# Kernel tuning notes

Hardware: AMD Instinct MI355X
Metric: run time of the kernel (lower is better)

The kernel has to match this reference:

```python
import jax, jax.numpy as jnp
import numpy as np

Tx, V, D = 512, 100, 64
DM, NH, DFF, NL = 512, 8, 2048, 2
H, DATT, FCH, OUT = 256, 128, 256, 2


def setup_inputs() -> dict:
    key = jax.random.key(0)
    ks = jax.random.split(key, 16)
    s = 0.02
    w = lambda k, shape: jax.random.normal(k, shape, jnp.float32) * s
    return dict(
        x_data=jax.random.normal(ks[0], (1, Tx, V, D), jnp.float32),
        feat_w=w(ks[1], (DM, D)), feat_b=jnp.zeros((DM,), jnp.float32),
        in_w=w(ks[2], (NL, 3 * DM, DM)), in_b=jnp.zeros((NL, 3 * DM), jnp.float32),
        out_w=w(ks[3], (NL, DM, DM)), out_b=jnp.zeros((NL, DM), jnp.float32),
        ff1_w=w(ks[4], (NL, DFF, DM)), ff1_b=jnp.zeros((NL, DFF), jnp.float32),
        ff2_w=w(ks[5], (NL, DM, DFF)), ff2_b=jnp.zeros((NL, DM), jnp.float32),
        ln1_g=jnp.ones((NL, DM), jnp.float32), ln1_b=jnp.zeros((NL, DM), jnp.float32),
        ln2_g=jnp.ones((NL, DM), jnp.float32), ln2_b=jnp.zeros((NL, DM), jnp.float32),
        att1_w=w(ks[6], (DATT, DM + H)), att1_b=jnp.zeros((DATT,), jnp.float32),
        att2_w=w(ks[7], (1, DATT)), att2_b=jnp.zeros((1,), jnp.float32),
        lstm_wih=w(ks[8], (4 * H, DM)), lstm_whh=w(ks[9], (4 * H, H)),
        lstm_bih=jnp.zeros((4 * H,), jnp.float32), lstm_bhh=jnp.zeros((4 * H,), jnp.float32),
        fc1_w=w(ks[10], (FCH, DM + H)), fc1_b=jnp.zeros((FCH,), jnp.float32),
        fc2_w=w(ks[11], (OUT, FCH)), fc2_b=jnp.zeros((OUT,), jnp.float32),
    )


def _layernorm(x, g, b):
    m = x.mean(-1, keepdims=True)
    v = x.var(-1, keepdims=True)
    return (x - m) * jax.lax.rsqrt(v + 1e-5) * g + b


def _forward(x_data, feat_w, feat_b, in_w, in_b, out_w, out_b, ff1_w, ff1_b,
             ff2_w, ff2_b, ln1_g, ln1_b, ln2_g, ln2_b, att1_w, att1_b,
             att2_w, att2_b, lstm_wih, lstm_whh, lstm_bih, lstm_bhh,
             fc1_w, fc1_b, fc2_w, fc2_b):
    x = x_data[0]                              # [Tx, V, D]
    x = jnp.swapaxes(x, 0, 1)                  # [V, Tx, D]  (seq=V, batch=Tx)
    x = x @ feat_w.T + feat_b                  # feature mapping -> [V, Tx, DM]
    # sinusoidal positional encoding over the V (seq) axis
    pos = jnp.arange(V, dtype=jnp.float32)[:, None]
    div = jnp.exp(jnp.arange(0, DM, 2, dtype=jnp.float32) * (-np.log(10000.0) / DM))
    pe = jnp.zeros((V, DM), jnp.float32)
    pe = pe.at[:, 0::2].set(jnp.sin(pos * div)).at[:, 1::2].set(jnp.cos(pos * div))
    x = x + pe[:, None, :]
    hd = DM // NH
    for l in range(NL):                        # post-norm TransformerEncoderLayer
        qkv = x @ in_w[l].T + in_b[l]          # [V, Tx, 3*DM]
        q, k, v = jnp.split(qkv, 3, axis=-1)
        q = q.reshape(V, Tx, NH, hd)
        k = k.reshape(V, Tx, NH, hd)
        v = v.reshape(V, Tx, NH, hd)
        scores = jnp.einsum('ibhd,jbhd->bhij', q, k) / np.sqrt(hd).astype(np.float32)
        attn = jax.nn.softmax(scores, axis=-1)
        ctx = jnp.einsum('bhij,jbhd->ibhd', attn, v).reshape(V, Tx, DM)
        x = _layernorm(x + ctx @ out_w[l].T + out_b[l], ln1_g[l], ln1_b[l])
        ff = jax.nn.relu(x @ ff1_w[l].T + ff1_b[l]) @ ff2_w[l].T + ff2_b[l]
        x = _layernorm(x + ff, ln2_g[l], ln2_b[l])
    hs = jnp.swapaxes(x, 0, 1)                 # [Tx, V, DM]

    def step(carry, h_i):                      # h_i: [V, DM]
        s_h, s_c = carry                       # [1, H] each
        att_in = jnp.concatenate([h_i, jnp.broadcast_to(s_h, (V, H))], axis=1)
        a1 = jnp.tanh(att_in @ att1_w.T + att1_b)
        a2 = a1 @ att2_w.T + att2_b            # [V, 1]
        a2 = a2 - jnp.max(a2)
        alpha = jnp.exp(a2)
        alpha = alpha / (jnp.sum(alpha, axis=0, keepdims=True) + 1e-15)
        c = jnp.sum(alpha * h_i, axis=0, keepdims=True)   # [1, DM]
        gates = c @ lstm_wih.T + lstm_bih + s_h @ lstm_whh.T + lstm_bhh
        i_g, f_g, g_g, o_g = jnp.split(gates, 4, axis=-1)
        s_c_new = jax.nn.sigmoid(f_g) * s_c + jax.nn.sigmoid(i_g) * jnp.tanh(g_g)
        s_h_new = jax.nn.sigmoid(o_g) * jnp.tanh(s_c_new)
        fc_in = jnp.concatenate([c, s_h], axis=1)  # uses PREVIOUS hidden, per original
        fc = jax.nn.relu(fc_in @ fc1_w.T + fc1_b) @ fc2_w.T + fc2_b
        log_prob = jax.nn.log_softmax(fc, axis=1)  # [1, OUT]
        return (s_h_new, s_c_new), log_prob

    init = (jnp.zeros((1, H), jnp.float32), jnp.zeros((1, H), jnp.float32))
    _, logs = jax.lax.scan(step, init, hs)
    return logs[-1]                            # last timestep's log-probs [1, OUT]


def reference(x_data, feat_w, feat_b, in_w, in_b, out_w, out_b, ff1_w, ff1_b,
              ff2_w, ff2_b, ln1_g, ln1_b, ln2_g, ln2_b, att1_w, att1_b,
              att2_w, att2_b, lstm_wih, lstm_whh, lstm_bih, lstm_bhh,
              fc1_w, fc1_b, fc2_w, fc2_b):
    return _forward(x_data, feat_w, feat_b, in_w, in_b, out_w, out_b, ff1_w,
                    ff1_b, ff2_w, ff2_b, ln1_g, ln1_b, ln2_g, ln2_b, att1_w,
                    att1_b, att2_w, att2_b, lstm_wih, lstm_whh, lstm_bih,
                    lstm_bhh, fc1_w, fc1_b, fc2_w, fc2_b)
```

## Files before the change

kernel.cpp:

```cpp
#include <hip/hip_runtime.h>
#include <hip/hip_bf16.h>


typedef __attribute__((ext_vector_type(8))) short short8;
typedef __attribute__((ext_vector_type(4))) float f32x4;

__device__ __forceinline__ int jglob_of(int e0, int jl) { return ((jl >> 4) << 8) + e0 + (jl & 15); }
__device__ __forceinline__ float blo(unsigned u) { return __uint_as_float(u << 16); }
__device__ __forceinline__ float bhi(unsigned u) { return __uint_as_float(u & 0xffff0000u); }
__device__ __forceinline__ short f2bs(float x) {
  union { __hip_bfloat16 h; short s; } u; u.h = __float2bfloat16(x); return u.s;
}
__device__ __forceinline__ float tanhf_fast(float x) {
  float e = __expf(2.f * x);
  return 1.f - 2.f * __builtin_amdgcn_rcpf(e + 1.f);
}

#define GLL16(GSRC, LDST) \
  __builtin_amdgcn_global_load_lds( \
      (const __attribute__((address_space(1))) unsigned int*)(GSRC), \
      (__attribute__((address_space(3))) unsigned int*)(LDST), 16, 0, 0)

__global__ __launch_bounds__(256) void pe_kernel(float* __restrict__ pe) {
  int idx = blockIdx.x * 256 + threadIdx.x;
  if (idx >= 100 * 512) return;
  int v = idx >> 9, n = idx & 511;
  float d = expf(-(float)(n & ~1) * (9.2103403719761836f / 512.0f));
  float ang = (float)v * d;
  pe[idx] = (n & 1) ? cosf(ang) : sinf(ang);
}

__global__ __launch_bounds__(256) void cvt2_kernel(const float* __restrict__ src,
                                                   __hip_bfloat16* __restrict__ dst,
                                                   int n, int w, int stride) {
  int i = blockIdx.x * 256 + threadIdx.x;
  if (i < n) dst[i] = __float2bfloat16(src[(i / w) * stride + (i % w)]);
}

__global__ __launch_bounds__(256) void gemm_bf16(
    const __hip_bfloat16* __restrict__ A, long aBase, int aDiv, long aSA, long aSB,
    const __hip_bfloat16* __restrict__ W, int ldw,
    const float* __restrict__ bias,
    float* __restrict__ outF, __hip_bfloat16* __restrict__ outB,
    long oBase, int oDiv, long oSA, long oSB, long oSC,
    int K, int addTo, int relu)
{
  __shared__ __hip_bfloat16 As[128 * 64];
  __shared__ __hip_bfloat16 Bs[128 * 64];
  const int tid = threadIdx.x;
  const int rT = blockIdx.y * 128, nT = blockIdx.x * 128;
  const int wave = tid >> 6, lane = tid & 63;
  const int wr = wave >> 1, wc = wave & 1;
  const int lrow = lane & 15, lkg = lane >> 4;

  long asrc[4], bsrc[4];
  const int sc8 = ((lane & 7) ^ (lane >> 3)) * 8;
#pragma unroll
  for (int i = 0; i < 4; ++i) {
    const int chunk = wave * 4 + i;
    const int row = chunk * 8 + (lane >> 3);
    const int gr = rT + row;
    asrc[i] = aBase + (long)(gr / aDiv) * aSA + (long)(gr % aDiv) * aSB + sc8;
    bsrc[i] = (long)(nT + row) * ldw + sc8;
  }

  f32x4 acc[4][4];
#pragma unroll
  for (int i = 0; i < 4; ++i)
#pragma unroll
    for (int j = 0; j < 4; ++j) acc[i][j] = (f32x4){0.f, 0.f, 0.f, 0.f};

  for (int k0 = 0; k0 < K; k0 += 64) {
#pragma unroll
    for (int i = 0; i < 4; ++i) {
      const int chunk = wave * 4 + i;
      GLL16(A + asrc[i] + k0, &As[chunk * 512]);
      GLL16(W + bsrc[i] + k0, &Bs[chunk * 512]);
    }
    __syncthreads();
#pragma unroll
    for (int ks = 0; ks < 2; ++ks) {
      short8 af[4], bfv[4];
#pragma unroll
      for (int f = 0; f < 4; ++f) {
        const int Ra = wr * 64 + f * 16 + lrow;
        af[f] = *(const short8*)&As[Ra * 64 + (((ks * 4 + lkg) ^ (Ra & 7)) * 8)];
        const int Rb = wc * 64 + f * 16 + lrow;
        bfv[f] = *(const short8*)&Bs[Rb * 64 + (((ks * 4 + lkg) ^ (Rb & 7)) * 8)];
      }
#pragma unroll
      for (int fm = 0; fm < 4; ++fm)
#pragma unroll
        for (int fn = 0; fn < 4; ++fn)
          acc[fm][fn] = __builtin_amdgcn_mfma_f32_16x16x32_bf16(af[fm], bfv[fn], acc[fm][fn], 0, 0, 0);
    }
    __syncthreads();
  }

  float bias_v[4];
#pragma unroll
  for (int fn = 0; fn < 4; ++fn)
    bias_v[fn] = bias ? bias[nT + wc * 64 + fn * 16 + lrow] : 0.f;

#pragma unroll
  for (int fm = 0; fm < 4; ++fm) {
#pragma unroll
    for (int r = 0; r < 4; ++r) {
      const int grow = rT + wr * 64 + fm * 16 + lkg * 4 + r;
      const long obase_r = oBase + (long)(grow / oDiv) * oSA + (long)(grow % oDiv) * oSB;
#pragma unroll
      for (int fn = 0; fn < 4; ++fn) {
        const int gcol = nT + wc * 64 + fn * 16 + lrow;
        float v = acc[fm][fn][r] + bias_v[fn];
        if (relu) v = fmaxf(v, 0.f);
        const long o = obase_r + (long)gcol * oSC;
        if (outF) { if (addTo) v += outF[o]; outF[o] = v; }
        else {
          if (addTo) v += __bfloat162float(outB[o]);
          outB[o] = __float2bfloat16(v);
        }
      }
    }
  }
}

__global__ __launch_bounds__(256) void gemm_mfma(
    const float* __restrict__ A, long aBase, int aDiv, long aSA, long aSB,
    const float* __restrict__ W, int ldw,
    const float* __restrict__ bias,
    const float* __restrict__ extra, int extraDiv,
    __hip_bfloat16* __restrict__ outB,
    long oBase, int oDiv, long oSA, long oSB,
    int N, int K)
{
  __shared__ short As[2][128][40];
  __shared__ short Bs[2][128][40];
  const int tid = threadIdx.x;
  const int rT = blockIdx.y * 128, nT = blockIdx.x * 128;
  const int wave = tid >> 6, lane = tid & 63;
  const int wr = wave >> 1, wc = wave & 1;
  const int lrow = lane & 15, lkg = lane >> 4;
  const int srow = tid >> 1, shf = tid & 1;

  const long arow = aBase + (long)((rT + srow) / aDiv) * aSA + (long)((rT + srow) % aDiv) * aSB + shf * 16;
  const long brow = (long)(nT + srow) * ldw + shf * 16;

  f32x4 acc[4][4];
#pragma unroll
  for (int i = 0; i < 4; ++i)
#pragma unroll
    for (int j = 0; j < 4; ++j) acc[i][j] = (f32x4){0.f, 0.f, 0.f, 0.f};

  float4 ra[4], rb[4];
#define LOADT(K0) do { \
    const float* _pa = A + arow + (K0); \
    ra[0] = *(const float4*)(_pa); ra[1] = *(const float4*)(_pa + 4); \
    ra[2] = *(const float4*)(_pa + 8); ra[3] = *(const float4*)(_pa + 12); \
    const float* _pb = W + brow + (K0); \
    rb[0] = *(const float4*)(_pb); rb[1] = *(const float4*)(_pb + 4); \
    rb[2] = *(const float4*)(_pb + 8); rb[3] = *(const float4*)(_pb + 12); \
  } while (0)

#define CVST(DST, X, Y) do { \
    short8 _v; \
    _v[0] = f2bs((X).x); _v[1] = f2bs((X).y); _v[2] = f2bs((X).z); _v[3] = f2bs((X).w); \
    _v[4] = f2bs((Y).x); _v[5] = f2bs((Y).y); _v[6] = f2bs((Y).z); _v[7] = f2bs((Y).w); \
    *(short8*)(DST) = _v; \
  } while (0)

#define STAGE(BUF) do { \
    CVST(&As[BUF][srow][shf * 16],     ra[0], ra[1]); \
    CVST(&As[BUF][srow][shf * 16 + 8], ra[2], ra[3]); \
    CVST(&Bs[BUF][srow][shf * 16],     rb[0], rb[1]); \
    CVST(&Bs[BUF][srow][shf * 16 + 8], rb[2], rb[3]); \
  } while (0)

  LOADT(0);
  STAGE(0);
  __syncthreads();

  int cur = 0;
  for (int k0 = 0; k0 < K; k0 += 32) {
    const bool nlast = (k0 + 32 < K);
    if (nlast) LOADT(k0 + 32);
    short8 af[4], bfv[4];
#pragma unroll
    for (int f = 0; f < 4; ++f)
      af[f] = *(const short8*)&As[cur][wr * 64 + f * 16 + lrow][lkg * 8];
#pragma unroll
    for (int f = 0; f < 4; ++f)
      bfv[f] = *(const short8*)&Bs[cur][wc * 64 + f * 16 + lrow][lkg * 8];
#pragma unroll
    for (int fm = 0; fm < 4; ++fm)
#pragma unroll
      for (int fn = 0; fn < 4; ++fn)
        acc[fm][fn] = __builtin_amdgcn_mfma_f32_16x16x32_bf16(af[fm], bfv[fn], acc[fm][fn], 0, 0, 0);
    if (nlast) STAGE(cur ^ 1);
    __syncthreads();
    cur ^= 1;
  }

  float bias_v[4];
#pragma unroll
  for (int fn = 0; fn < 4; ++fn)
    bias_v[fn] = bias ? bias[nT + wc * 64 + fn * 16 + lrow] : 0.f;

#pragma unroll
  for (int fm = 0; fm < 4; ++fm) {
#pragma unroll
    for (int r = 0; r < 4; ++r) {
      const int grow = rT + wr * 64 + fm * 16 + lkg * 4 + r;
      const long obase_r = oBase + (long)(grow / oDiv) * oSA + (long)(grow % oDiv) * oSB;
      const long exrow = (long)(grow / extraDiv) * N;
#pragma unroll
      for (int fn = 0; fn < 4; ++fn) {
        const int gcol = nT + wc * 64 + fn * 16 + lrow;
        float v = acc[fm][fn][r] + bias_v[fn];
        if (extra) v += extra[exrow + gcol];
        outB[obase_r + gcol] = __float2bfloat16(v);
      }
    }
  }
#undef LOADT
#undef CVST
#undef STAGE
}

__global__ __launch_bounds__(256) void attn_kernel(
    const __hip_bfloat16* __restrict__ qkv, __hip_bfloat16* __restrict__ outY, int b0)
{
  __shared__ __align__(16) char arena[101632];
  unsigned short* Qs = (unsigned short*)arena;
  unsigned short* Ks = Qs + 8064;
  unsigned short* Vt = Ks + 8064;
  float* S = (float*)(arena + 49664);
  unsigned short* Sb = (unsigned short*)arena;
  __shared__ float rs_s[112];

  const int h = blockIdx.x, bl = blockIdx.y, tid = threadIdx.x;
  const unsigned short* q16 = (const unsigned short*)qkv;

  for (int idx = tid; idx < 6400; idx += 256) {
    int v = idx >> 6, d = idx & 63;
    long base = ((long)(v * 256 + bl)) * 1536 + h * 64 + d;
    Qs[v * 72 + d] = q16[base];
    Ks[v * 72 + d] = q16[base + 512];
    Vt[d * 136 + v] = q16[base + 1024];
  }
  for (int idx = tid; idx < 12 * 64; idx += 256) {
    int r = 100 + (idx >> 6), c = idx & 63;
    Qs[r * 72 + c] = 0; Ks[r * 72 + c] = 0;
  }
  for (int idx = tid; idx < 64 * 36; idx += 256) {
    int d = idx / 36, c = 100 + idx % 36;
    Vt[d * 136 + c] = 0;
  }
  __syncthreads();

  const int wave = tid >> 6, lane = tid & 63;
  const int lrow = lane & 15, lkg = lane >> 4;

  for (int tt = wave; tt < 49; tt += 4) {
    const int tm = tt / 7, tn = tt % 7;
    f32x4 a = (f32x4){0.f, 0.f, 0.f, 0.f};
#pragma unroll
    for (int ks = 0; ks < 2; ++ks) {
      short8 af = *(const short8*)&Qs[(tm * 16 + lrow) * 72 + ks * 32 + lkg * 8];
      short8 bf = *(const short8*)&Ks[(tn * 16 + lrow) * 72 + ks * 32 + lkg * 8];
      a = __builtin_amdgcn_mfma_f32_16x16x32_bf16(af, bf, a, 0, 0, 0);
    }
#pragma unroll
    for (int r = 0; r < 4; ++r)
      S[(tm * 16 + lkg * 4 + r) * 116 + tn * 16 + lrow] = a[r] * 0.125f;
  }
  __syncthreads();

  {
    unsigned* p = (unsigned*)Sb;
    for (int idx = tid; idx < 7616; idx += 256) p[idx] = 0;
  }
  __syncthreads();

  if (tid < 200) {
    const int r = tid >> 1, hf = tid & 1;
    const float* srow = S + r * 116 + hf * 50;
    float m = -3.0e38f;
    for (int c = 0; c < 50; ++c) m = fmaxf(m, srow[c]);
    m = fmaxf(m, __shfl_xor(m, 1, 64));
    float s = 0.f;
    for (int c = 0; c < 50; ++c) {
      float e = __expf(srow[c] - m);
      Sb[r * 136 + hf * 50 + c] = (unsigned short)f2bs(e);
      s += e;
    }
    s += __shfl_xor(s, 1, 64);
    if (hf == 0) rs_s[r] = 1.f / s;
  }
  __syncthreads();

  for (int tt = wave; tt < 28; tt += 4) {
    const int tm = tt >> 2, tn = tt & 3;
    f32x4 a = (f32x4){0.f, 0.f, 0.f, 0.f};
#pragma unroll
    for (int kc = 0; kc < 4; ++kc) {
      short8 af = *(const short8*)&Sb[(tm * 16 + lrow) * 136 + kc * 32 + lkg * 8];
      short8 bf = *(const short8*)&Vt[(tn * 16 + lrow) * 136 + kc * 32 + lkg * 8];
      a = __builtin_amdgcn_mfma_f32_16x16x32_bf16(af, bf, a, 0, 0, 0);
    }
#pragma unroll
    for (int r = 0; r < 4; ++r) {
      const int m = tm * 16 + lkg * 4 + r;
      if (m < 100) {
        const int n = tn * 16 + lrow;
        outY[((long)(m * 512 + b0 + bl)) * 512 + h * 64 + n] = __float2bfloat16(a[r] * rs_s[m]);
      }
    }
  }
}

__global__ __launch_bounds__(256) void ln_kernel(__hip_bfloat16* __restrict__ X,
    const float* __restrict__ g, const float* __restrict__ b)
{
  const int row = blockIdx.x * 4 + (threadIdx.x >> 6);
  const int lane = threadIdx.x & 63;
  unsigned short* x = (unsigned short*)X + (long)row * 512 + lane * 8;
  uint4 raw = *(const uint4*)x;
  float v[8];
  v[0] = blo(raw.x); v[1] = bhi(raw.x); v[2] = blo(raw.y); v[3] = bhi(raw.y);
  v[4] = blo(raw.z); v[5] = bhi(raw.z); v[6] = blo(raw.w); v[7] = bhi(raw.w);
  float s = 0.f, sq = 0.f;
#pragma unroll
  for (int i = 0; i < 8; ++i) { s += v[i]; sq += v[i] * v[i]; }
#pragma unroll
  for (int off = 32; off; off >>= 1) { s += __shfl_xor(s, off, 64); sq += __shfl_xor(sq, off, 64); }
  const float mean = s * (1.f / 512.f);
  const float var = sq * (1.f / 512.f) - mean * mean;
  const float inv = rsqrtf(var + 1e-5f);
  const int c0 = lane * 8;
  short8 outv;
#pragma unroll
  for (int i = 0; i < 8; ++i)
    outv[i] = f2bs((v[i] - mean) * inv * g[c0 + i] + b[c0 + i]);
  *(short8*)x = outv;
}

__global__ void init_kernel(unsigned long long* sh_units, float* c_g) {
  int t = threadIdx.x;
  sh_units[t] = 0ULL;
  sh_units[256 + t] = 0ULL;
  c_g[t] = 0.f; c_g[256 + t] = 0.f;
}

#define DEC_NB 16

__global__ __launch_bounds__(256, 1) void decoder_kernel(
    const __hip_bfloat16* __restrict__ Xb,
    const __hip_bfloat16* __restrict__ Pb,
    const __hip_bfloat16* __restrict__ Gb,
    const float* __restrict__ att1_w, const float* __restrict__ att1_b,
    const float* __restrict__ att2_w,
    const float* __restrict__ whh,
    const float* __restrict__ bih, const float* __restrict__ bhh,
    const float* __restrict__ fc1_w, const float* __restrict__ fc1_b,
    const float* __restrict__ fc2_w, const float* __restrict__ fc2_b,
    unsigned long long* sh_units,
    float* c_g,
    float* __restrict__ out)
{
  if (blockIdx.x & 7) return;
  const int tid = threadIdx.x;
  const int blk = blockIdx.x >> 3;
  const int e0 = blk * 16;

  __shared__ __align__(16) float s_h_s[256];
  __shared__ float w2_s[128], ub_s[128], bsum_s[64];
  __shared__ float u_s[128], sc_s[16];
  __shared__ float a2_s[104];
  __shared__ float red_s[256];
  __shared__ float gates_s[64];
  __shared__ float red4_s[4];
  __shared__ float fcin_s[768];
  __shared__ float fca_s[256];

  if (tid < 128) { w2_s[tid] = att2_w[tid]; ub_s[tid] = att1_b[tid]; }
  if (tid < 64) {
    int jg = jglob_of(e0, tid);
    bsum_s[tid] = bih[jg] + bhh[jg];
  }
  if (tid < 16) sc_s[tid] = 0.f;
  if (tid < 4) a2_s[100 + tid] = 0.f;

  const int pv = tid >> 1, ppart = tid & 1;
  const int pvv = (pv < 100) ? pv : 99;
  const int gjl = tid >> 2, gq = tid & 3;
  const long gRowOff = (long)jglob_of(e0, gjl) * 100 + gq * 26;

  unsigned W1R[64];
  {
    const int j = tid >> 1, hf = tid & 1;
    const float* wsrc = att1_w + (long)j * 768 + 512 + hf * 128;
#pragma unroll
    for (int i = 0; i < 64; ++i)
      W1R[i] = (unsigned)(unsigned short)f2bs(wsrc[2 * i]) |
               ((unsigned)(unsigned short)f2bs(wsrc[2 * i + 1]) << 16);
  }
  float WHF[64];
  {
    const float* wsrc = whh + (long)jglob_of(e0, gjl) * 256 + gq * 64;
#pragma unroll
    for (int i = 0; i < 64; ++i) WHF[i] = wsrc[i];
  }

  unsigned PCa[32], PCb[32];
  unsigned GCa[13], GCb[13];

#define PREFETCH(T1, PCd, GCd) do { \
    const uint4* _pp = (const uint4*)Pb + ((((long)(T1) * 100 + pvv) * 128 + ppart * 64) >> 3); \
    _Pragma("unroll") \
    for (int _i = 0; _i < 8; ++_i) { \
      uint4 _t = _pp[_i]; \
      (PCd)[4*_i] = _t.x; (PCd)[4*_i+1] = _t.y; (PCd)[4*_i+2] = _t.z; (PCd)[4*_i+3] = _t.w; \
    } \
    const unsigned* _gp = (const unsigned*)(Gb + (long)(T1) * 102400 + gRowOff); \
    _Pragma("unroll") \
    for (int _i = 0; _i < 13; ++_i) (GCd)[_i] = _gp[_i]; \
  } while (0)

#define STEP(T, PCc, GCc, PCn, GCn) do { \
    { \
      unsigned long long* _up = &sh_units[((((T) & 1) ^ 1) << 8) + tid]; \
      unsigned long long _v = __hip_atomic_load(_up, __ATOMIC_RELAXED, __HIP_MEMORY_SCOPE_AGENT); \
      while ((unsigned)(_v >> 32) < (unsigned)(T)) { \
        __builtin_amdgcn_s_sleep(1); \
        _v = __hip_atomic_load(_up, __ATOMIC_RELAXED, __HIP_MEMORY_SCOPE_AGENT); \
      } \
      s_h_s[tid] = __uint_as_float((unsigned)_v); \
    } \
    __syncthreads(); \
    if ((T) + 1 < 512) PREFETCH((T) + 1, PCn, GCn); \
    { const int _hf = tid & 1, _j = tid >> 1; \
      const float* _sh = &s_h_s[_hf * 128]; \
      float _a = 0.f; \
      _Pragma("unroll") \
      for (int _i = 0; _i < 64; ++_i) { \
        const unsigned _w = W1R[_i]; \
        const float2 _s2 = *(const float2*)(_sh + 2 * _i); \
        _a += blo(_w) * _s2.x + bhi(_w) * _s2.y; \
      } \
      _a += __shfl_xor(_a, 1, 64); \
      if (_hf == 0) u_s[_j] = _a + ub_s[_j]; \
    } \
    float _hhv; \
    { const float* _sh = &s_h_s[gq * 64]; \
      float _a = 0.f; \
      _Pragma("unroll") \
      for (int _i = 0; _i < 16; ++_i) { \
        const float4 _s4 = *(const float4*)(_sh + 4 * _i); \
        _a += WHF[4*_i] * _s4.x + WHF[4*_i+1] * _s4.y + WHF[4*_i+2] * _s4.z + WHF[4*_i+3] * _s4.w; \
      } \
      _a += __shfl_xor(_a, 1, 64); \
      _a += __shfl_xor(_a, 2, 64); \
      _hhv = _a; \
    } \
    __syncthreads(); \
    { float _val = 0.f; \
      _Pragma("unroll") \
      for (int _jj = 0; _jj < 64; ++_jj) { \
        unsigned _u = (PCc)[_jj >> 1]; \
        float _pf = (_jj & 1) ? bhi(_u) : blo(_u); \
        int _col = ppart * 64 + _jj; \
        _val += tanhf_fast(_pf + u_s[_col]) * w2_s[_col]; \
      } \
      _val += __shfl_xor(_val, 1, 64); \
      if (ppart == 0 && pv < 100) a2_s[pv] = _val; \
    } \
    __syncthreads(); \
    if (tid < 64) { \
      float _x0 = a2_s[tid]; \
      float _x1 = (tid + 64 < 100) ? a2_s[tid + 64] : -3.0e38f; \
      float _m = fmaxf(_x0, _x1); \
      _Pragma("unroll") \
      for (int _o = 32; _o; _o >>= 1) _m = fmaxf(_m, __shfl_xor(_m, _o, 64)); \
      float _e0 = __expf(_x0 - _m); \
      float _e1 = (tid + 64 < 100) ? __expf(_x1 - _m) : 0.f; \
      float _s = _e0 + _e1; \
      _Pragma("unroll") \
      for (int _o = 32; _o; _o >>= 1) _s += __shfl_xor(_s, _o, 64); \
      const float _inv = 1.f / (_s + 1e-15f); \
      a2_s[tid] = _e0 * _inv; \
      if (tid + 64 < 100) a2_s[tid + 64] = _e1 * _inv; \
    } \
    __syncthreads(); \
    { float _p = 0.f; \
      _Pragma("unroll") \
      for (int _i = 0; _i < 13; ++_i) { \
        unsigned _u = (GCc)[_i]; \
        _p += a2_s[gq * 26 + 2 * _i] * blo(_u); \
        _p += a2_s[gq * 26 + 2 * _i + 1] * bhi(_u); \
      } \
      _p += __shfl_xor(_p, 1, 64); \
      _p += __shfl_xor(_p, 2, 64); \
      if (gq == 0) gates_s[gjl] = _p + _hhv + bsum_s[gjl]; \
    } \
    __syncthreads(); \
    if ((T) < 511) { \
      if (tid < 16) { \
        const float _ig = gates_s[tid], _fg = gates_s[16 + tid]; \
        const float _gg = gates_s[32 + tid], _og = gates_s[48 + tid]; \
        const float _si = 1.f / (1.f + __expf(-_ig)); \
        const float _sf = 1.f / (1.f + __expf(-_fg)); \
        const float _so = 1.f / (1.f + __expf(-_og)); \
        const float _sc = _sf * sc_s[tid] + _si * tanhf(_gg); \
        sc_s[tid] = _sc; \
        const float _sh2 = _so * tanhf(_sc); \
        const unsigned long long _v = \
            ((unsigned long long)(unsigned)((T) + 1) << 32) | (unsigned long long)__float_as_uint(_sh2); \
        __hip_atomic_store(&sh_units[(((T) & 1) << 8) + e0 + tid], _v, \
                           __ATOMIC_RELAXED, __HIP_MEMORY_SCOPE_AGENT); \
      } \
    } else { \
      const int _dl = tid & 31, _vs = tid >> 5; \
      const int _v0 = _vs * 13, _v1 = (_v0 + 13 < 100) ? _v0 + 13 : 100; \
      float _ac = 0.f; \
      for (int _v = _v0; _v < _v1; ++_v) \
        _ac += a2_s[_v] * __bfloat162float(Xb[((long)(_v * 512 + 511)) * 512 + blk * 32 + _dl]); \
      red_s[tid] = _ac; \
      __syncthreads(); \
      if (tid < 32) { \
        float _cc = 0.f; \
        _Pragma("unroll") \
        for (int _s = 0; _s < 8; ++_s) _cc += red_s[_s * 32 + tid]; \
        __hip_atomic_store(&c_g[blk * 32 + tid], _cc, __ATOMIC_RELAXED, __HIP_MEMORY_SCOPE_AGENT); \
      } \
      __syncthreads(); \
      if (tid == 0) \
        __hip_atomic_store(&sh_units[256 + e0], 512ULL << 32, \
                           __ATOMIC_RELEASE, __HIP_MEMORY_SCOPE_AGENT); \
    } \
  } while (0)

  PREFETCH(0, PCa, GCa);
  __syncthreads();

  for (int t2 = 0; t2 < 512; t2 += 2) {
    STEP(t2,     PCa, GCa, PCb, GCb);
    STEP(t2 + 1, PCb, GCb, PCa, GCa);
  }

  if (blk == 0) {
    if (tid < DEC_NB) {
      while ((unsigned)(__hip_atomic_load(&sh_units[256 + tid * 16],
                 __ATOMIC_RELAXED, __HIP_MEMORY_SCOPE_AGENT) >> 32) < 512u)
        __builtin_amdgcn_s_sleep(1);
    }
    __builtin_amdgcn_fence(__ATOMIC_ACQUIRE, "agent");
    __syncthreads();
    fcin_s[tid]       = __hip_atomic_load(&c_g[tid],       __ATOMIC_RELAXED, __HIP_MEMORY_SCOPE_AGENT);
    fcin_s[256 + tid] = __hip_atomic_load(&c_g[256 + tid], __ATOMIC_RELAXED, __HIP_MEMORY_SCOPE_AGENT);
    fcin_s[512 + tid] = s_h_s[tid];
    __syncthreads();
    float acc = fc1_b[tid];
    const float* w = fc1_w + (long)tid * 768;
    for (int k = 0; k < 768; ++k) acc += w[k] * fcin_s[k];
    fca_s[tid] = fmaxf(acc, 0.f);
    __syncthreads();
    if (tid < 128) {
      const int r = tid >> 6, k0 = tid & 63;
      float a = 0.f;
#pragma unroll
      for (int s = 0; s < 4; ++s) a += fc2_w[r * 256 + k0 + s * 64] * fca_s[k0 + s * 64];
#pragma unroll
      for (int off = 32; off; off >>= 1) a += __shfl_xor(a, off, 64);
      if (k0 == 0) red4_s[r] = a + fc2_b[r];
    }
    __syncthreads();
    if (tid == 0) {
      const float l0 = red4_s[0], l1 = red4_s[1];
      const float m = fmaxf(l0, l1);
      const float ls = logf(__expf(l0 - m) + __expf(l1 - m));
      out[0] = l0 - m - ls;
      out[1] = l1 - m - ls;
    }
  }
#undef PREFETCH
#undef STEP
}

extern "C" void kernel_launch(void* const* d_in, const int* in_sizes, int n_in,
                              void* d_out, int out_size, void* d_ws, size_t ws_size,
                              hipStream_t stream) {
  const float* x_data  = (const float*)d_in[0];
  const float* feat_w  = (const float*)d_in[1];
  const float* feat_b  = (const float*)d_in[2];
  const float* in_w    = (const float*)d_in[3];
  const float* in_b    = (const float*)d_in[4];
  const float* out_w   = (const float*)d_in[5];
  const float* out_b   = (const float*)d_in[6];
  const float* ff1_w   = (const float*)d_in[7];
  const float* ff1_b   = (const float*)d_in[8];
  const float* ff2_w   = (const float*)d_in[9];
  const float* ff2_b   = (const float*)d_in[10];
  const float* ln1_g   = (const float*)d_in[11];
  const float* ln1_b   = (const float*)d_in[12];
  const float* ln2_g   = (const float*)d_in[13];
  const float* ln2_b   = (const float*)d_in[14];
  const float* att1_w  = (const float*)d_in[15];
  const float* att1_b  = (const float*)d_in[16];
  const float* att2_w  = (const float*)d_in[17];
  const float* lstm_wih = (const float*)d_in[19];
  const float* lstm_whh = (const float*)d_in[20];
  const float* lstm_bih = (const float*)d_in[21];
  const float* lstm_bhh = (const float*)d_in[22];
  const float* fc1_w   = (const float*)d_in[23];
  const float* fc1_b   = (const float*)d_in[24];
  const float* fc2_w   = (const float*)d_in[25];
  const float* fc2_b   = (const float*)d_in[26];

  float* ws   = (float*)d_ws;
  __hip_bfloat16* Xb = (__hip_bfloat16*)ws;
  float* R2   = ws + 13107200;
  __hip_bfloat16* qkvb = (__hip_bfloat16*)R2;
  __hip_bfloat16* ctxb = (__hip_bfloat16*)(R2 + 19660800);
  __hip_bfloat16* ffh  = (__hip_bfloat16*)R2;
  __hip_bfloat16* PbB  = (__hip_bfloat16*)R2;
  __hip_bfloat16* GbB  = (__hip_bfloat16*)(R2 + 3276800);
  __hip_bfloat16* wbp  = (__hip_bfloat16*)(R2 + 32768000);
  __hip_bfloat16* in_wb  = wbp;
  __hip_bfloat16* out_wb = wbp + 1572864;
  __hip_bfloat16* ff1_wb = wbp + 2097152;
  __hip_bfloat16* ff2_wb = wbp + 4194304;
  __hip_bfloat16* att1c  = wbp + 6291456;
  __hip_bfloat16* wih_b  = wbp + 6356992;
  float* pe    = R2 + 32768000 + 3440640;
  unsigned long long* sh_units = (unsigned long long*)(pe + 51200);
  float* c_g   = (float*)(sh_units + 512);

  pe_kernel<<<200, 256, 0, stream>>>(pe);
  cvt2_kernel<<<(1572864 + 255) / 256, 256, 0, stream>>>(in_w, in_wb, 1572864, 512, 512);
  cvt2_kernel<<<(524288 + 255) / 256, 256, 0, stream>>>(out_w, out_wb, 524288, 512, 512);
  cvt2_kernel<<<(2097152 + 255) / 256, 256, 0, stream>>>(ff1_w, ff1_wb, 2097152, 512, 512);
  cvt2_kernel<<<(2097152 + 255) / 256, 256, 0, stream>>>(ff2_w, ff2_wb, 2097152, 2048, 2048);
  cvt2_kernel<<<(65536 + 255) / 256, 256, 0, stream>>>(att1_w, att1c, 65536, 512, 768);
  cvt2_kernel<<<(524288 + 255) / 256, 256, 0, stream>>>(lstm_wih, wih_b, 524288, 512, 512);

  gemm_mfma<<<dim3(4, 400), 256, 0, stream>>>(
      x_data, 0L, 512, 64L, 6400L, feat_w, 64, feat_b, pe, 512,
      Xb, 0L, 1 << 30, 0L, 512L, 512, 64);

  for (int l = 0; l < 2; ++l) {
    for (int c = 0; c < 2; ++c) {
      const long b0 = c * 256;
      gemm_bf16<<<dim3(12, 200), 256, 0, stream>>>(
          Xb, b0 * 512, 256, 262144L, 512L,
          in_wb + (long)l * 786432, 512, in_b + l * 1536,
          nullptr, qkvb, 0L, 1 << 30, 0L, 1536L, 1L, 512, 0, 0);
      attn_kernel<<<dim3(8, 256), 256, 0, stream>>>(qkvb, ctxb, (int)b0);
    }
    gemm_bf16<<<dim3(4, 400), 256, 0, stream>>>(
        ctxb, 0L, 1 << 30, 0L, 512L,
        out_wb + (long)l * 262144, 512, out_b + l * 512,
        nullptr, Xb, 0L, 1 << 30, 0L, 512L, 1L, 512, 1, 0);
    ln_kernel<<<12800, 256, 0, stream>>>(Xb, ln1_g + l * 512, ln1_b + l * 512);
    for (int rc = 0; rc < 2; ++rc) {
      const long r0 = (long)rc * 25600;
      gemm_bf16<<<dim3(16, 200), 256, 0, stream>>>(
          Xb, r0 * 512, 1 << 30, 0L, 512L,
          ff1_wb + (long)l * 1048576, 512, ff1_b + l * 2048,
          nullptr, ffh, 0L, 1 << 30, 0L, 2048L, 1L, 512, 0, 1);
      gemm_bf16<<<dim3(4, 200), 256, 0, stream>>>(
          ffh, 0L, 1 << 30, 0L, 2048L,
          ff2_wb + (long)l * 1048576, 2048, ff2_b + l * 512,
          nullptr, Xb, r0 * 512, 1 << 30, 0L, 512L, 1L, 2048, 1, 0);
    }
    ln_kernel<<<12800, 256, 0, stream>>>(Xb, ln2_g + l * 512, ln2_b + l * 512);
  }

  gemm_bf16<<<dim3(1, 400), 256, 0, stream>>>(
      Xb, 0L, 100, 512L, 262144L, att1c, 512, nullptr,
      nullptr, PbB, 0L, 1 << 30, 0L, 128L, 1L, 512, 0, 0);
  gemm_bf16<<<dim3(8, 400), 256, 0, stream>>>(
      Xb, 0L, 100, 512L, 262144L, wih_b, 512, nullptr,
      nullptr, GbB, 0L, 100, 102400L, 1L, 100L, 512, 0, 0);

  init_kernel<<<1, 256, 0, stream>>>(sh_units, c_g);
  decoder_kernel<<<DEC_NB * 8, 256, 0, stream>>>(
      Xb, PbB, GbB, att1_w, att1_b, att2_w,
      lstm_whh, lstm_bih, lstm_bhh, fc1_w, fc1_b, fc2_w, fc2_b,
      sh_units, c_g, (float*)d_out);
}
```

Before: 4.884 ms.

## Merge weight conversion and PE kernels; store LSTM input gates row-major

Replaces seven small prep launches (positional encoding plus six fp32-to-bf16 weight conversions) with a single combined kernel, which removes launch overhead. It also changes the layout of the LSTM input-gate GEMM output from [t][gate][v] to [t][v][gate]. The decoder now gathers 26 separate bf16 values per thread with a stride of 1024 instead of 13 contiguous 32-bit loads. That stride makes the decoder loads less contiguous per thread, though adjacent threads may coalesce across gates, and the GEMM epilogue writes become contiguous.

Result: slower. 5.548 ms (+13.6%).

```diff
diff --git a/kernel.cpp b/kernel.cpp
--- a/kernel.cpp
+++ b/kernel.cpp
@@ -21,20 +21,29 @@
       (const __attribute__((address_space(1))) unsigned int*)(GSRC), \
       (__attribute__((address_space(3))) unsigned int*)(LDST), 16, 0, 0)
 
-__global__ __launch_bounds__(256) void pe_kernel(float* __restrict__ pe) {
-  int idx = blockIdx.x * 256 + threadIdx.x;
-  if (idx >= 100 * 512) return;
-  int v = idx >> 9, n = idx & 511;
-  float d = expf(-(float)(n & ~1) * (9.2103403719761836f / 512.0f));
-  float ang = (float)v * d;
-  pe[idx] = (n & 1) ? cosf(ang) : sinf(ang);
-}
-
-__global__ __launch_bounds__(256) void cvt2_kernel(const float* __restrict__ src,
-                                                   __hip_bfloat16* __restrict__ dst,
-                                                   int n, int w, int stride) {
+__global__ __launch_bounds__(256) void prep_kernel(
+    const float* __restrict__ in_w, const float* __restrict__ out_w,
+    const float* __restrict__ ff1_w, const float* __restrict__ ff2_w,
+    const float* __restrict__ att1_w, const float* __restrict__ wih,
+    __hip_bfloat16* __restrict__ dst, float* __restrict__ pe)
+{
   int i = blockIdx.x * 256 + threadIdx.x;
-  if (i < n) dst[i] = __float2bfloat16(src[(i / w) * stride + (i % w)]);
+  if (i < 6881280) {
+    const float* s; long off;
+    if (i < 1572864)      { s = in_w;  off = i; }
+    else if (i < 2097152) { s = out_w; off = i - 1572864; }
+    else if (i < 4194304) { s = ff1_w; off = i - 2097152; }
+    else if (i < 6291456) { s = ff2_w; off = i - 4194304; }
+    else if (i < 6356992) { int k = i - 6291456; s = att1_w; off = (long)(k >> 9) * 768 + (k & 511); }
+    else                  { s = wih;   off = i - 6356992; }
+    dst[i] = __float2bfloat16(s[off]);
+  } else if (i < 6881280 + 51200) {
+    int idx = i - 6881280;
+    int v = idx >> 9, n = idx & 511;
+    float d = expf(-(float)(n & ~1) * (9.2103403719761836f / 512.0f));
+    float ang = (float)v * d;
+    pe[idx] = (n & 1) ? cosf(ang) : sinf(ang);
+  }
 }
 
 __global__ __launch_bounds__(256) void gemm_bf16(
@@ -393,7 +402,7 @@
   const int pv = tid >> 1, ppart = tid & 1;
   const int pvv = (pv < 100) ? pv : 99;
   const int gjl = tid >> 2, gq = tid & 3;
-  const long gRowOff = (long)jglob_of(e0, gjl) * 100 + gq * 26;
+  const int jgG = jglob_of(e0, gjl);
 
   unsigned W1R[64];
   {
@@ -412,7 +421,7 @@
   }
 
   unsigned PCa[32], PCb[32];
-  unsigned GCa[13], GCb[13];
+  unsigned short GCa[26], GCb[26];
 
 #define PREFETCH(T1, PCd, GCd) do { \
     const uint4* _pp = (const uint4*)Pb + ((((long)(T1) * 100 + pvv) * 128 + ppart * 64) >> 3); \
@@ -421,9 +430,12 @@
       uint4 _t = _pp[_i]; \
       (PCd)[4*_i] = _t.x; (PCd)[4*_i+1] = _t.y; (PCd)[4*_i+2] = _t.z; (PCd)[4*_i+3] = _t.w; \
     } \
-    const unsigned* _gp = (const unsigned*)(Gb + (long)(T1) * 102400 + gRowOff); \
+    const unsigned short* _gs = (const unsigned short*)Gb + (long)(T1) * 102400 + jgG; \
     _Pragma("unroll") \
-    for (int _i = 0; _i < 13; ++_i) (GCd)[_i] = _gp[_i]; \
+    for (int _i = 0; _i < 26; ++_i) { \
+      int _v = gq * 26 + _i; if (_v > 99) _v = 99; \
+      (GCd)[_i] = _gs[(long)_v * 1024]; \
+    } \
   } while (0)
 
 #define STEP(T, PCc, GCc, PCn, GCn) do { \
@@ -493,11 +505,8 @@
     __syncthreads(); \
     { float _p = 0.f; \
       _Pragma("unroll") \
-      for (int _i = 0; _i < 13; ++_i) { \
-        unsigned _u = (GCc)[_i]; \
-        _p += a2_s[gq * 26 + 2 * _i] * blo(_u); \
-        _p += a2_s[gq * 26 + 2 * _i + 1] * bhi(_u); \
-      } \
+      for (int _i = 0; _i < 26; ++_i) \
+        _p += a2_s[gq * 26 + _i] * blo((unsigned)(GCc)[_i]); \
       _p += __shfl_xor(_p, 1, 64); \
       _p += __shfl_xor(_p, 2, 64); \
       if (gq == 0) gates_s[gjl] = _p + _hhv + bsum_s[gjl]; \
@@ -635,13 +644,8 @@
   unsigned long long* sh_units = (unsigned long long*)(pe + 51200);
   float* c_g   = (float*)(sh_units + 512);
 
-  pe_kernel<<<200, 256, 0, stream>>>(pe);
-  cvt2_kernel<<<(1572864 + 255) / 256, 256, 0, stream>>>(in_w, in_wb, 1572864, 512, 512);
-  cvt2_kernel<<<(524288 + 255) / 256, 256, 0, stream>>>(out_w, out_wb, 524288, 512, 512);
-  cvt2_kernel<<<(2097152 + 255) / 256, 256, 0, stream>>>(ff1_w, ff1_wb, 2097152, 512, 512);
-  cvt2_kernel<<<(2097152 + 255) / 256, 256, 0, stream>>>(ff2_w, ff2_wb, 2097152, 2048, 2048);
-  cvt2_kernel<<<(65536 + 255) / 256, 256, 0, stream>>>(att1_w, att1c, 65536, 512, 768);
-  cvt2_kernel<<<(524288 + 255) / 256, 256, 0, stream>>>(lstm_wih, wih_b, 524288, 512, 512);
+  prep_kernel<<<(6881280 + 51200 + 255) / 256, 256, 0, stream>>>(
+      in_w, out_w, ff1_w, ff2_w, att1_w, lstm_wih, wbp, pe);
 
   gemm_mfma<<<dim3(4, 400), 256, 0, stream>>>(
       x_data, 0L, 512, 64L, 6400L, feat_w, 64, feat_b, pe, 512,
@@ -680,7 +684,7 @@
       nullptr, PbB, 0L, 1 << 30, 0L, 128L, 1L, 512, 0, 0);
   gemm_bf16<<<dim3(8, 400), 256, 0, stream>>>(
       Xb, 0L, 100, 512L, 262144L, wih_b, 512, nullptr,
-      nullptr, GbB, 0L, 100, 102400L, 1L, 100L, 512, 0, 0);
+      nullptr, GbB, 0L, 1 << 30, 0L, 1024L, 1L, 512, 0, 0);
 
   init_kernel<<<1, 256, 0, stream>>>(sh_units, c_g);
   decoder_kernel<<<DEC_NB * 8, 256, 0, stream>>>(
```
